# Kernel tuning notes

Measured on AMD Instinct MI355X. Metric: run time of the kernel, lower is better.

Reference implementation:

```python
import jax, jax.numpy as jnp
import numpy as np

N = 1024   # num nodes (assets)
F = 128    # node feature dim (node_dim)
M = 256    # memory_dim (scorer hidden)
E = 8      # edge_dim
BN_EPS = 1e-5


def setup_inputs() -> dict:
    key = jax.random.key(0)
    ks = jax.random.split(key, 6)
    x = jax.random.normal(ks[0], (N, F), dtype=jnp.float32)
    ctx = jax.random.uniform(ks[1], (4,), dtype=jnp.float32)  # [crisis_prob, ttc/30, urgency, confidence]
    W1 = jax.random.normal(ks[2], (M, 2 * F + 4), dtype=jnp.float32) * 0.05
    b1 = jnp.zeros((M,), jnp.float32)
    gamma = jnp.ones((M,), jnp.float32)
    beta = jnp.zeros((M,), jnp.float32)
    run_mean = jnp.zeros((M,), jnp.float32)
    run_var = jnp.ones((M,), jnp.float32)
    W2 = jax.random.normal(ks[3], (E, M), dtype=jnp.float32) * 0.05
    b2 = jnp.zeros((E,), jnp.float32)
    W3 = jax.random.normal(ks[4], (1, E), dtype=jnp.float32) * 0.05
    b3 = jnp.zeros((1,), jnp.float32)
    return {"x": x, "ctx": ctx, "W1": W1, "b1": b1, "gamma": gamma, "beta": beta,
            "run_mean": run_mean, "run_var": run_var, "W2": W2, "b2": b2, "W3": W3, "b3": b3}


def reference(x, ctx, W1, b1, gamma, beta, run_mean, run_var, W2, b2, W3, b3):
    # All unordered pairs i<j (static shapes); original loops over stressed pairs only,
    # we score all pairs and expose the stressed/threshold filter as a boolean mask.
    ii, jj = jnp.triu_indices(N, k=1)  # each [P], P = N*(N-1)/2

    # First linear decomposed: W1 @ [x_i; x_j; ctx] = A x_i + B x_j + (C ctx + b1)
    pa = x @ W1[:, :F].T          # [N, M]
    pb = x @ W1[:, F:2 * F].T     # [N, M]
    cterm = ctx @ W1[:, 2 * F:].T + b1  # [M]

    h = jax.nn.relu(pa[ii] + pb[jj] + cterm)                           # [P, M]
    h = gamma * (h - run_mean) * jax.lax.rsqrt(run_var + BN_EPS) + beta  # eval-mode BatchNorm1d
    h = jax.nn.relu(h @ W2.T + b2)                                     # [P, E]
    scores = jax.nn.sigmoid(h @ W3.T + b3)[:, 0]                       # [P]

    # Stressed-node selection: std over feature dim > mean std (torch unbiased std)
    stress = x.std(axis=1, ddof=1)
    stressed = stress > stress.mean()
    edge_mask = (scores > 0.5) & stressed[ii] & stressed[jj]           # [P] bool
    return scores, edge_mask
```

## Files before the change

kernel.cpp:

```cpp
#include <hip/hip_runtime.h>
#include <math.h>

#define N_NODES 1024
#define F_DIM   128
#define M_DIM   256
#define E_DIM   8
#define P_PAIRS 523776
#define NBLK    1056

__global__ __launch_bounds__(256) void kA(const float* __restrict__ x,
                                          const float* __restrict__ ctx,
                                          const float* __restrict__ W1,
                                          const float* __restrict__ b1,
                                          const float* __restrict__ gamma,
                                          const float* __restrict__ beta,
                                          const float* __restrict__ rmean,
                                          const float* __restrict__ rvar,
                                          const float* __restrict__ W2,
                                          const float* __restrict__ b2,
                                          float* __restrict__ pa,
                                          float* __restrict__ pb,
                                          float* __restrict__ stress,
                                          float* __restrict__ w2ft,
                                          float* __restrict__ b2f) {
  const int t = threadIdx.x;

  if (blockIdx.x == 256) {
    __shared__ float bnbs[256];
    const float s   = gamma[t] / sqrtf(rvar[t] + 1e-5f);
    bnbs[t] = beta[t] - s * rmean[t];
    #pragma unroll
    for (int e = 0; e < 8; ++e) w2ft[t * 8 + e] = W2[e * 256 + t] * s;
    __syncthreads();
    const int wv = t >> 6, lane = t & 63;
    #pragma unroll
    for (int r = 0; r < 2; ++r) {
      const int e = wv * 2 + r;
      float acc = 0.f;
      #pragma unroll
      for (int k = 0; k < 4; ++k) acc += W2[e * 256 + lane + 64 * k] * bnbs[lane + 64 * k];
      #pragma unroll
      for (int m = 32; m > 0; m >>= 1) acc += __shfl_xor(acc, m, 64);
      if (lane == 0) b2f[e] = acc + b2[e];
    }
    return;
  }

  __shared__ float xv[4][128];
  const int n0 = blockIdx.x * 4;
  if (t < 128) {
    ((float4*)&xv[0][0])[t] = ((const float4*)(x + (size_t)n0 * F_DIM))[t];
  }
  __syncthreads();

  {
    const int wv = t >> 6, lane = t & 63;
    const float a = xv[wv][lane], b = xv[wv][lane + 64];
    float sum = a + b;
    #pragma unroll
    for (int m = 32; m > 0; m >>= 1) sum += __shfl_xor(sum, m, 64);
    const float mean = sum * (1.0f / 128.0f);
    const float d0 = a - mean, d1 = b - mean;
    float ss = d0 * d0 + d1 * d1;
    #pragma unroll
    for (int m = 32; m > 0; m >>= 1) ss += __shfl_xor(ss, m, 64);
    if (lane == 0) stress[n0 + wv] = sqrtf(ss * (1.0f / 127.0f));
  }

  const int m = t;
  const float4* wrow = (const float4*)(W1 + (size_t)m * 260);
  float accA[4] = {0.f, 0.f, 0.f, 0.f};
  float accB[4] = {0.f, 0.f, 0.f, 0.f};
  #pragma unroll 8
  for (int k4 = 0; k4 < 32; ++k4) {
    const float4 wa = wrow[k4];
    const float4 wb = wrow[32 + k4];
    #pragma unroll
    for (int nn = 0; nn < 4; ++nn) {
      const float4 xf = ((const float4*)&xv[nn][0])[k4];
      accA[nn] = fmaf(xf.w, wa.w, fmaf(xf.z, wa.z, fmaf(xf.y, wa.y, fmaf(xf.x, wa.x, accA[nn]))));
      accB[nn] = fmaf(xf.w, wb.w, fmaf(xf.z, wb.z, fmaf(xf.y, wb.y, fmaf(xf.x, wb.x, accB[nn]))));
    }
  }
  const float c0 = ctx[0], c1 = ctx[1], c2 = ctx[2], c3 = ctx[3];
  const float* rowt = W1 + (size_t)m * 260 + 256;
  const float ctv = b1[m] + c0 * rowt[0] + c1 * rowt[1] + c2 * rowt[2] + c3 * rowt[3];
  #pragma unroll
  for (int nn = 0; nn < 4; ++nn) {
    pa[(size_t)(n0 + nn) * M_DIM + m] = accA[nn] + ctv;
    pb[(size_t)(n0 + nn) * M_DIM + m] = accB[nn];
  }
}

__global__ __launch_bounds__(256, 4) void kC(const float* __restrict__ pa,
                                             const float* __restrict__ pb,
                                             const float* __restrict__ w2ft,
                                             const float* __restrict__ b2f,
                                             const float* __restrict__ W3,
                                             const float* __restrict__ b3,
                                             const float* __restrict__ stress,
                                             float* __restrict__ out) {
  __shared__ float4 a4[16 * 32];
  __shared__ float4 b4[32 * 32];
  const int t = threadIdx.x;

  const int p = blockIdx.x;
  int tj = (int)((sqrtf(4.0f * (float)p + 1.0f) - 1.0f) * 0.5f);
  while ((tj + 1) * (tj + 2) <= p) ++tj;
  while (tj * (tj + 1) > p) --tj;
  const int si = p - tj * (tj + 1);
  const int i0 = si * 16, j0 = tj * 32;

  float ssum = 0.f;
  {
    const int lane = t & 63;
    #pragma unroll
    for (int k = 0; k < 16; ++k) ssum += stress[lane + 64 * k];
    #pragma unroll
    for (int m = 32; m > 0; m >>= 1) ssum += __shfl_xor(ssum, m, 64);
  }
  const float smean = ssum * (1.0f / 1024.0f);

  const int jx = t & 15;
  const int iy = t >> 4;
  float acc[2][8];
  #pragma unroll
  for (int q = 0; q < 2; ++q)
    #pragma unroll
    for (int e = 0; e < 8; ++e) acc[q][e] = 0.f;

  const float4* pa4 = (const float4*)pa;
  const float4* pb4 = (const float4*)pb;
  const float4* w4g = (const float4*)w2ft;

  float4 rg[6];

  #pragma unroll
  for (int q = 0; q < 6; ++q) {
    const int d = q * 256 + t;
    if (q < 2) {
      const int r = d >> 5, dc = d & 31, c = (dc - r) & 31;
      rg[q] = pa4[(size_t)(i0 + r) * 64 + c];
    } else {
      const int d2 = d - 512, r = d2 >> 5, dc = d2 & 31, c = (dc - r) & 31;
      rg[q] = pb4[(size_t)(j0 + r) * 64 + c];
    }
  }
  #pragma unroll
  for (int q = 0; q < 6; ++q) {
    const int d = q * 256 + t;
    if (q < 2) a4[d] = rg[q]; else b4[d - 512] = rg[q];
  }
  __syncthreads();

  #pragma unroll
  for (int q = 0; q < 6; ++q) {
    const int d = q * 256 + t;
    if (q < 2) {
      const int r = d >> 5, dc = d & 31, c = (dc - r) & 31;
      rg[q] = pa4[(size_t)(i0 + r) * 64 + 32 + c];
    } else {
      const int d2 = d - 512, r = d2 >> 5, dc = d2 & 31, c = (dc - r) & 31;
      rg[q] = pb4[(size_t)(j0 + r) * 64 + 32 + c];
    }
  }

  auto computeChunk = [&](int cw) {
    float4 wc[8], wn[8];
    #pragma unroll
    for (int q = 0; q < 8; ++q) wc[q] = w4g[cw * 8 + q];
    for (int m4 = 0; m4 < 32; ++m4) {
      if (m4 < 31) {
        #pragma unroll
        for (int q = 0; q < 8; ++q) wn[q] = w4g[(cw + m4 + 1) * 8 + q];
      }
      const float4 a0 = a4[iy * 32        + ((m4 + iy) & 31)];
      const float4 b0 = b4[jx * 32        + ((m4 + jx) & 31)];
      const float4 b1 = b4[(jx + 16) * 32 + ((m4 + jx + 16) & 31)];
      const float* a0f = (const float*)&a0;
      const float* b0f = (const float*)&b0;
      const float* b1f = (const float*)&b1;
      #pragma unroll
      for (int mm = 0; mm < 4; ++mm) {
        const float r0 = fmaxf(a0f[mm] + b0f[mm], 0.f);
        const float r1 = fmaxf(a0f[mm] + b1f[mm], 0.f);
        const float* wl = (const float*)&wc[mm * 2];
        const float* wh = (const float*)&wc[mm * 2 + 1];
        #pragma unroll
        for (int e = 0; e < 4; ++e) {
          acc[0][e]     = fmaf(wl[e], r0, acc[0][e]);
          acc[1][e]     = fmaf(wl[e], r1, acc[1][e]);
          acc[0][e + 4] = fmaf(wh[e], r0, acc[0][e + 4]);
          acc[1][e + 4] = fmaf(wh[e], r1, acc[1][e + 4]);
        }
      }
      #pragma unroll
      for (int q = 0; q < 8; ++q) wc[q] = wn[q];
    }
  };

  computeChunk(0);
  __syncthreads();
  #pragma unroll
  for (int q = 0; q < 6; ++q) {
    const int d = q * 256 + t;
    if (q < 2) a4[d] = rg[q]; else b4[d - 512] = rg[q];
  }
  __syncthreads();
  computeChunk(32);

  float w3v[8], b2v[8];
  #pragma unroll
  for (int e = 0; e < 8; ++e) { w3v[e] = W3[e]; b2v[e] = b2f[e]; }
  const float b3v = b3[0];
  const int i = i0 + iy;
  #pragma unroll
  for (int jb = 0; jb < 2; ++jb) {
    const int j = j0 + jx + jb * 16;
    if (i < j) {
      float logit = b3v;
      #pragma unroll
      for (int e = 0; e < 8; ++e) {
        const float h2 = fmaxf(acc[jb][e] + b2v[e], 0.f);
        logit = fmaf(w3v[e], h2, logit);
      }
      const float score = 1.0f / (1.0f + expf(-logit));
      const int idx = i * 1023 - (i * (i - 1)) / 2 + (j - i - 1);
      out[idx] = score;
      const bool mk = (score > 0.5f) && (stress[i] > smean) && (stress[j] > smean);
      out[P_PAIRS + idx] = mk ? 1.0f : 0.0f;
    }
  }
}

extern "C" void kernel_launch(void* const* d_in, const int* in_sizes, int n_in,
                              void* d_out, int out_size, void* d_ws, size_t ws_size,
                              hipStream_t stream) {
  const float* x     = (const float*)d_in[0];
  const float* ctx   = (const float*)d_in[1];
  const float* W1    = (const float*)d_in[2];
  const float* b1    = (const float*)d_in[3];
  const float* gamma = (const float*)d_in[4];
  const float* beta  = (const float*)d_in[5];
  const float* rmean = (const float*)d_in[6];
  const float* rvar  = (const float*)d_in[7];
  const float* W2    = (const float*)d_in[8];
  const float* b2    = (const float*)d_in[9];
  const float* W3    = (const float*)d_in[10];
  const float* b3    = (const float*)d_in[11];
  float* out = (float*)d_out;

  float* ws     = (float*)d_ws;
  float* pa     = ws;
  float* pb     = pa + 262144;
  float* w2ft   = pb + 262144;
  float* b2f    = w2ft + 2048;
  float* stress = b2f + 8;

  hipLaunchKernelGGL(kA, dim3(257), dim3(256), 0, stream, x, ctx, W1, b1, gamma, beta,
                     rmean, rvar, W2, b2, pa, pb, stress, w2ft, b2f);
  hipLaunchKernelGGL(kC, dim3(NBLK), dim3(256), 0, stream, pa, pb, w2ft, b2f,
                     W3, b3, stress, out);
}
```

Before: 129.9 us.

## Use packed FMA, padded LDS pitch, and drop manual weight prefetch in pair kernel

```diff
diff --git a/kernel.cpp b/kernel.cpp
--- a/kernel.cpp
+++ b/kernel.cpp
@@ -7,6 +7,24 @@
 #define E_DIM   8
 #define P_PAIRS 523776
 #define NBLK    1056
+#define APITCH  33
+
+typedef float v2f __attribute__((ext_vector_type(2)));
+
+#if defined(__has_builtin)
+#if __has_builtin(__builtin_elementwise_fma)
+#define PK_FMA(a, b, c) __builtin_elementwise_fma((a), (b), (c))
+#endif
+#endif
+#ifndef PK_FMA
+static __device__ inline v2f pk_fma_fallback(v2f a, v2f b, v2f c) {
+  v2f r;
+  r.x = fmaf(a.x, b.x, c.x);
+  r.y = fmaf(a.y, b.y, c.y);
+  return r;
+}
+#define PK_FMA(a, b, c) pk_fma_fallback((a), (b), (c))
+#endif
 
 __global__ __launch_bounds__(256) void kA(const float* __restrict__ x,
                                           const float* __restrict__ ctx,
@@ -67,8 +85,7 @@
     if (lane == 0) stress[n0 + wv] = sqrtf(ss * (1.0f / 127.0f));
   }
 
-  const int m = t;
-  const float4* wrow = (const float4*)(W1 + (size_t)m * 260);
+  const float4* wrow = (const float4*)(W1 + (size_t)t * 260);
   float accA[4] = {0.f, 0.f, 0.f, 0.f};
   float accB[4] = {0.f, 0.f, 0.f, 0.f};
   #pragma unroll 8
@@ -83,12 +100,12 @@
     }
   }
   const float c0 = ctx[0], c1 = ctx[1], c2 = ctx[2], c3 = ctx[3];
-  const float* rowt = W1 + (size_t)m * 260 + 256;
-  const float ctv = b1[m] + c0 * rowt[0] + c1 * rowt[1] + c2 * rowt[2] + c3 * rowt[3];
+  const float* rowt = W1 + (size_t)t * 260 + 256;
+  const float ctv = b1[t] + c0 * rowt[0] + c1 * rowt[1] + c2 * rowt[2] + c3 * rowt[3];
   #pragma unroll
   for (int nn = 0; nn < 4; ++nn) {
-    pa[(size_t)(n0 + nn) * M_DIM + m] = accA[nn] + ctv;
-    pb[(size_t)(n0 + nn) * M_DIM + m] = accB[nn];
+    pa[(size_t)(n0 + nn) * M_DIM + t] = accA[nn] + ctv;
+    pb[(size_t)(n0 + nn) * M_DIM + t] = accB[nn];
   }
 }
 
@@ -100,8 +117,8 @@
                                              const float* __restrict__ b3,
                                              const float* __restrict__ stress,
                                              float* __restrict__ out) {
-  __shared__ float4 a4[16 * 32];
-  __shared__ float4 b4[32 * 32];
+  __shared__ float4 a4[16 * APITCH];
+  __shared__ float4 b4[32 * APITCH];
   const int t = threadIdx.x;
 
   const int p = blockIdx.x;
@@ -123,11 +140,11 @@
 
   const int jx = t & 15;
   const int iy = t >> 4;
-  float acc[2][8];
+  v2f acc[2][4];
   #pragma unroll
   for (int q = 0; q < 2; ++q)
     #pragma unroll
-    for (int e = 0; e < 8; ++e) acc[q][e] = 0.f;
+    for (int k = 0; k < 4; ++k) acc[q][k] = (v2f){0.f, 0.f};
 
   const float4* pa4 = (const float4*)pa;
   const float4* pb4 = (const float4*)pb;
@@ -137,46 +154,51 @@
 
   #pragma unroll
   for (int q = 0; q < 6; ++q) {
-    const int d = q * 256 + t;
-    if (q < 2) {
-      const int r = d >> 5, dc = d & 31, c = (dc - r) & 31;
+    if (q < 2) {
+      const int d = q * 256 + t, r = d >> 5, c = d & 31;
       rg[q] = pa4[(size_t)(i0 + r) * 64 + c];
     } else {
-      const int d2 = d - 512, r = d2 >> 5, dc = d2 & 31, c = (dc - r) & 31;
+      const int d2 = (q - 2) * 256 + t, r = d2 >> 5, c = d2 & 31;
       rg[q] = pb4[(size_t)(j0 + r) * 64 + c];
     }
   }
   #pragma unroll
   for (int q = 0; q < 6; ++q) {
-    const int d = q * 256 + t;
-    if (q < 2) a4[d] = rg[q]; else b4[d - 512] = rg[q];
-  }
-  __syncthreads();
-
-  #pragma unroll
-  for (int q = 0; q < 6; ++q) {
-    const int d = q * 256 + t;
-    if (q < 2) {
-      const int r = d >> 5, dc = d & 31, c = (dc - r) & 31;
+    if (q < 2) {
+      const int d = q * 256 + t, r = d >> 5, c = d & 31;
+      a4[r * APITCH + c] = rg[q];
+    } else {
+      const int d2 = (q - 2) * 256 + t, r = d2 >> 5, c = d2 & 31;
+      b4[r * APITCH + c] = rg[q];
+    }
+  }
+  __syncthreads();
+
+  #pragma unroll
+  for (int q = 0; q < 6; ++q) {
+    if (q < 2) {
+      const int d = q * 256 + t, r = d >> 5, c = d & 31;
       rg[q] = pa4[(size_t)(i0 + r) * 64 + 32 + c];
     } else {
-      const int d2 = d - 512, r = d2 >> 5, dc = d2 & 31, c = (dc - r) & 31;
+      const int d2 = (q - 2) * 256 + t, r = d2 >> 5, c = d2 & 31;
       rg[q] = pb4[(size_t)(j0 + r) * 64 + 32 + c];
     }
   }
 
+  const float4* aRow  = a4 + iy * APITCH;
+  const float4* bRow0 = b4 + jx * APITCH;
+  const float4* bRow1 = b4 + (jx + 16) * APITCH;
+
   auto computeChunk = [&](int cw) {
-    float4 wc[8], wn[8];
-    #pragma unroll
-    for (int q = 0; q < 8; ++q) wc[q] = w4g[cw * 8 + q];
+    #pragma unroll 4
     for (int m4 = 0; m4 < 32; ++m4) {
-      if (m4 < 31) {
-        #pragma unroll
-        for (int q = 0; q < 8; ++q) wn[q] = w4g[(cw + m4 + 1) * 8 + q];
-      }
-      const float4 a0 = a4[iy * 32        + ((m4 + iy) & 31)];
-      const float4 b0 = b4[jx * 32        + ((m4 + jx) & 31)];
-      const float4 b1 = b4[(jx + 16) * 32 + ((m4 + jx + 16) & 31)];
+      const float4 a0 = aRow[m4];
+      const float4 b0 = bRow0[m4];
+      const float4 b1 = bRow1[m4];
+      float4 wc[8];
+      #pragma unroll
+      for (int q = 0; q < 8; ++q) wc[q] = w4g[(cw + m4) * 8 + q];
+
       const float* a0f = (const float*)&a0;
       const float* b0f = (const float*)&b0;
       const float* b1f = (const float*)&b1;
@@ -184,18 +206,15 @@
       for (int mm = 0; mm < 4; ++mm) {
         const float r0 = fmaxf(a0f[mm] + b0f[mm], 0.f);
         const float r1 = fmaxf(a0f[mm] + b1f[mm], 0.f);
-        const float* wl = (const float*)&wc[mm * 2];
-        const float* wh = (const float*)&wc[mm * 2 + 1];
+        const v2f rr0 = {r0, r0};
+        const v2f rr1 = {r1, r1};
+        const v2f* wp = (const v2f*)&wc[mm * 2];
         #pragma unroll
-        for (int e = 0; e < 4; ++e) {
-          acc[0][e]     = fmaf(wl[e], r0, acc[0][e]);
-          acc[1][e]     = fmaf(wl[e], r1, acc[1][e]);
-          acc[0][e + 4] = fmaf(wh[e], r0, acc[0][e + 4]);
-          acc[1][e + 4] = fmaf(wh[e], r1, acc[1][e + 4]);
+        for (int k = 0; k < 4; ++k) {
+          acc[0][k] = PK_FMA(wp[k], rr0, acc[0][k]);
+          acc[1][k] = PK_FMA(wp[k], rr1, acc[1][k]);
         }
       }
-      #pragma unroll
-      for (int q = 0; q < 8; ++q) wc[q] = wn[q];
     }
   };
 
@@ -203,8 +222,13 @@
   __syncthreads();
   #pragma unroll
   for (int q = 0; q < 6; ++q) {
-    const int d = q * 256 + t;
-    if (q < 2) a4[d] = rg[q]; else b4[d - 512] = rg[q];
+    if (q < 2) {
+      const int d = q * 256 + t, r = d >> 5, c = d & 31;
+      a4[r * APITCH + c] = rg[q];
+    } else {
+      const int d2 = (q - 2) * 256 + t, r = d2 >> 5, c = d2 & 31;
+      b4[r * APITCH + c] = rg[q];
+    }
   }
   __syncthreads();
   computeChunk(32);
@@ -218,10 +242,11 @@
   for (int jb = 0; jb < 2; ++jb) {
     const int j = j0 + jx + jb * 16;
     if (i < j) {
+      const float* af = (const float*)&acc[jb][0];
       float logit = b3v;
       #pragma unroll
       for (int e = 0; e < 8; ++e) {
-        const float h2 = fmaxf(acc[jb][e] + b2v[e], 0.f);
+        const float h2 = fmaxf(af[e] + b2v[e], 0.f);
         logit = fmaf(w3v[e], h2, logit);
       }
       const float score = 1.0f / (1.0f + expf(-logit));
```

Result: faster. 124.4 us (-4.2%).
